# Kernel tuning notes

Hardware: AMD Instinct MI355X
Metric: run time of the kernel (lower is better)

Reference implementation:

```python
import jax, jax.numpy as jnp
import numpy as np

C = 32           # in_channels
KH, KW = 3, 3    # kernel_range
SHIFT = 1
NP = KH * KW


def conv2d(x, w, b, pad):
    # x: NCHW, w: OIHW
    y = jax.lax.conv_general_dilated(
        x, w, window_strides=(1, 1), padding=[(pad, pad), (pad, pad)],
        dimension_numbers=('NCHW', 'OIHW', 'NCHW'))
    return y + b[None, :, None, None]


def setup_inputs() -> dict:
    key = jax.random.key(0)
    ks = jax.random.split(key, 14)
    p = lambda k, shape: (jax.random.normal(k, shape, dtype=jnp.float32) * 0.02)
    inp = {
        'x':  jax.random.normal(ks[0], (4, C, 256, 256), dtype=jnp.float32),
        'wk': p(ks[1], (C * NP, C, 1, 1)), 'bk': p(ks[2], (C * NP,)),
        'wv': p(ks[3], (C * NP, C, 1, 1)), 'bv': p(ks[4], (C * NP,)),
        'wq': p(ks[5], (C, C, 1, 1)),      'bq': p(ks[6], (C,)),
        'w1': p(ks[7], (C, C, 3, 3)),      'b1': p(ks[8], (C,)),
        'w2': p(ks[9], (2 * C, C, 3, 3)),  'b2': p(ks[10], (2 * C,)),
        'w3': p(ks[11], (C, 2 * C, 3, 3)), 'b3': p(ks[12], (C,)),
    }
    return inp


def reference(x, wk, bk, wv, bv, wq, bq, w1, b1, w2, b2, w3, b3):
    B, D, H, W = x.shape
    h_half, w_half = KH // 2, KW // 2
    ph, pw = h_half * SHIFT, w_half * SHIFT

    x_k = conv2d(x, wk, bk, 0)  # (B, D*NP, H, W)
    x_v = conv2d(x, wv, bv, 0)
    x_q = conv2d(x, wq, bq, 0)  # (B, D, H, W)

    pad4 = ((0, 0), (0, 0), (ph, ph), (pw, pw))
    x_k = jnp.pad(x_k, pad4)
    x_v = jnp.pad(x_v, pad4)
    mask_pad = jnp.pad(jnp.ones((B, 1, H, W), x.dtype), pad4)

    k_ls, v_ls, m_ls = [], [], []
    layer = 0
    for i in range(-h_half, h_half + 1):
        for j in range(-w_half, w_half + 1):
            r0 = ph + i * SHIFT
            c0 = pw + j * SHIFT
            k_ls.append(x_k[:, layer * D:(layer + 1) * D, r0:r0 + H, c0:c0 + W])
            v_ls.append(x_v[:, layer * D:(layer + 1) * D, r0:r0 + H, c0:c0 + W])
            m_ls.append(mask_pad[:, :, r0:r0 + H, c0:c0 + W])
            layer += 1

    # Faithful to torch .view semantics: flat row-major reshape, NOT a permute.
    k = jnp.stack(k_ls, axis=1).reshape(B * H * W, NP, D)   # (B,NP,D,H,W) -> flat
    v = jnp.stack(v_ls, axis=1).reshape(B * H * W, NP, D)
    m = jnp.stack(m_ls, axis=1).reshape(B * H * W, NP, 1)
    q = x_q.reshape(B * H * W, 1, D)                         # (B,D,H,W) -> flat

    scores = jnp.matmul(k, jnp.swapaxes(q, -1, -2)) * m / 8.0  # (N, NP, 1)
    alpha = jax.nn.softmax(scores, axis=1)
    res = jnp.matmul(jnp.swapaxes(alpha, -1, -2), v)           # (N, 1, D)
    t = res.reshape(B, D, H, W)

    t = jax.nn.relu(conv2d(t, w1, b1, 1))
    t = jax.nn.relu(conv2d(t, w2, b2, 1))
    t = jax.nn.relu(conv2d(t, w3, b3, 1))
    return t
```

## Files before the change

### kernel.cpp

```cpp
#include <hip/hip_runtime.h>
#include <hip/hip_bf16.h>

#define B_ 4
#define C_ 32
#define H_ 256
#define W_ 256
#define S_ 65536
#define NP_ 9
#define OC_ 288
#define PR 258
#define PWN 264

using bf16 = __hip_bfloat16;
typedef __attribute__((ext_vector_type(8)))  short  short8;
typedef __attribute__((ext_vector_type(4)))  short  short4_t;
typedef __attribute__((ext_vector_type(16))) float  f32x16;

__device__ __forceinline__ float b2f(short s) {
    return __uint_as_float(((unsigned)(unsigned short)s) << 16);
}

template<int IC, int OC>
__device__ __forceinline__ void prepA_body(int fid, const float* __restrict__ w,
                                           bf16* __restrict__ apk)
{
    constexpr int NK = 9 * IC / 16;
    int tile = fid >> 9;
    int l = (fid >> 3) & 63;
    int j = fid & 7;
    int mt = tile / NK;
    int ks = tile - mt * NK;
    int q = l >> 5;
    int oc = mt * 32 + (l & 31);
    int k = ks * 16 + q * 8 + j;
    int tap = k / IC;
    int ic = k - tap * IC;
    apk[fid] = __float2bfloat16(w[((oc * IC + ic) * 3 + tap / 3) * 3 + tap % 3]);
}

template<int G>
__device__ __forceinline__ void zerob_body(int b, int p, uint4* __restrict__ buf)
{
    int gran;
    if (p < 2 * PWN * G) {
        int row = (p < PWN * G) ? 0 : 257;
        int rem = p % (PWN * G);
        gran = row * PWN * G + rem;
    } else {
        int p2 = p - 2 * PWN * G;
        int col = (p2 < 256 * G) ? 0 : 257;
        int rem = p2 % (256 * G);
        int r = rem / G + 1;
        int icg = rem - (rem / G) * G;
        gran = (r * PWN + col) * G + icg;
    }
    buf[(size_t)b * PR * PWN * G + gran] = uint4{0, 0, 0, 0};
}

__global__ __launch_bounds__(256) void k_prep(
    const float* __restrict__ wk, const float* __restrict__ wv,
    const float* __restrict__ wq,
    const float* __restrict__ w1, const float* __restrict__ w2,
    const float* __restrict__ w3,
    bf16* __restrict__ apk0, bf16* __restrict__ apk1,
    bf16* __restrict__ apk2, bf16* __restrict__ apk3,
    uint4* __restrict__ tA, uint4* __restrict__ t1, uint4* __restrict__ t2)
{
    int idx = blockIdx.x * 256 + threadIdx.x;
    if (idx < 19456) {
        int j    = idx & 7;
        int lane = (idx >> 3) & 63;
        int ks   = (idx >> 9) & 1;
        int mt   = idx >> 10;
        int oc = lane & 31;
        int ic = ks * 16 + (lane >> 5) * 8 + j;
        const float* w; int ocg;
        if (mt < 9)       { w = wk; ocg = mt * 32 + oc; }
        else if (mt < 18) { w = wv; ocg = (mt - 9) * 32 + oc; }
        else              { w = wq; ocg = oc; }
        apk0[idx] = __float2bfloat16(w[ocg * C_ + ic]);
    } else if (idx < 28672) {
        prepA_body<32, 32>(idx - 19456, w1, apk1);
    } else if (idx < 47104) {
        prepA_body<32, 64>(idx - 28672, w2, apk2);
    } else if (idx < 65536) {
        prepA_body<64, 32>(idx - 47104, w3, apk3);
    } else if (idx < 82176) {
        int i5 = idx - 65536;
        zerob_body<4>(i5 / 4160, i5 % 4160, tA);
    } else if (idx < 98816) {
        int i6 = idx - 82176;
        zerob_body<4>(i6 / 4160, i6 % 4160, t1);
    } else if (idx < 132096) {
        int i7 = idx - 98816;
        zerob_body<8>(i7 / 8320, i7 % 8320, t2);
    }
}

__global__ __launch_bounds__(256) void k_q(
    const float* __restrict__ x, const bf16* __restrict__ apk,
    const float* __restrict__ bq, bf16* __restrict__ xq)
{
    __shared__ bf16 lbuf[32][140];
    int bh  = blockIdx.x >> 9;
    int blk = blockIdx.x & 511;
    int pixw0 = blk << 7;
    int tid  = threadIdx.x;
    int wvi  = tid >> 6;
    int lane = tid & 63;
    int col  = lane & 31, q = lane >> 5;
    int pix  = pixw0 + wvi * 32 + col;

    const float* xb = x + (size_t)bh * (C_ * S_);
    bf16* xqb = xq + (size_t)bh * (32 * S_);

    short8 bfrag[2];
#pragma unroll
    for (int kk = 0; kk < 2; ++kk)
#pragma unroll
        for (int j = 0; j < 8; ++j) {
            bf16 h = __float2bfloat16(xb[(size_t)(kk * 16 + q * 8 + j) * S_ + pix]);
            bfrag[kk][j] = *reinterpret_cast<short*>(&h);
        }

    const short8* apkv = reinterpret_cast<const short8*>(apk);
    f32x16 acc = {};
    acc = __builtin_amdgcn_mfma_f32_32x32x16_bf16(bfrag[0], apkv[(18 * 2 + 0) * 64 + lane], acc, 0, 0, 0);
    acc = __builtin_amdgcn_mfma_f32_32x32x16_bf16(bfrag[1], apkv[(18 * 2 + 1) * 64 + lane], acc, 0, 0, 0);
    float bbv = bq[col];
#pragma unroll
    for (int g4 = 0; g4 < 4; ++g4) {
        short4_t sv;
#pragma unroll
        for (int j = 0; j < 4; ++j) {
            bf16 hb = __float2bfloat16(acc[g4 * 4 + j] + bbv);
            sv[j] = *reinterpret_cast<short*>(&hb);
        }
        *reinterpret_cast<short4_t*>(&lbuf[col][wvi * 32 + 8 * g4 + 4 * q]) = sv;
    }
    __syncthreads();
    int ch0 = tid >> 4, chk = tid & 15, ch1 = ch0 + 16;
    short8 v0 = *reinterpret_cast<const short8*>(&lbuf[ch0][chk * 8]);
    *reinterpret_cast<short8*>(xqb + (size_t)ch0 * S_ + pixw0 + chk * 8) = v0;
    short8 v1 = *reinterpret_cast<const short8*>(&lbuf[ch1][chk * 8]);
    *reinterpret_cast<short8*>(xqb + (size_t)ch1 * S_ + pixw0 + chk * 8) = v1;
}


#define DO_TILE(T, DTOT)                                                              \
{                                                                                     \
    int Tg = (s0 >> 5) + (T);                                                         \
    unsigned n = (unsigned)plane_base + ((unsigned)Tg << 5);                          \
    unsigned tl = (n >> 5) / 9u;                               \
    int sk0 = (int)(tl * 288u) - plane_base;                                          \
    const bf16* qp = xqb + ((size_t)tl << 5) + 4 * q;                                 \
    short4_t q0 = *reinterpret_cast<const short4_t*>(qp);                             \
    short4_t q1 = *reinterpret_cast<const short4_t*>(qp + 8);                         \
    short4_t q2 = *reinterpret_cast<const short4_t*>(qp + 16);                        \
    short4_t q3 = *reinterpret_cast<const short4_t*>(qp + 24);                        \
    int xib = ((T) << 5) + 257 + di * 256 + dj + col;                                 \
    int swx = (xib ^ (xib >> 2)) & 3;                                                 \
    short8 fa = *reinterpret_cast<const short8*>(&xs[xib * 4 + (q ^ swx)]);           \
    short8 fb = *reinterpret_cast<const short8*>(&xs[xib * 4 + ((2 + q) ^ swx)]);     \
    f32x16 ka = (f32x16){}, vh = (f32x16){};                                          \
    ka = __builtin_amdgcn_mfma_f32_32x32x16_bf16(fa, apkv[(p * 2 + 0) * 64 + lane], ka, 0, 0, 0); \
    ka = __builtin_amdgcn_mfma_f32_32x32x16_bf16(fb, apkv[(p * 2 + 1) * 64 + lane], ka, 0, 0, 0); \
    vh = __builtin_amdgcn_mfma_f32_32x32x16_bf16(fa, apkv[((9 + p) * 2 + 0) * 64 + lane], vh, 0, 0, 0); \
    vh = __builtin_amdgcn_mfma_f32_32x32x16_bf16(fb, apkv[((9 + p) * 2 + 1) * 64 + lane], vh, 0, 0, 0); \
    bool hbad  = (32 * (T) < hb_lo) || (32 * (T) >= hb_hi);                           \
    bool tb_lo = (dj == -1) && ((Tg & 7) == 0);                                       \
    bool tb_hi = (dj == 1) && ((Tg & 7) == 7);                                        \
    if (tb_lo && q == 0) q0[0] = 0;                       \
    if (tb_hi && q == 1) q3[3] = 0;                      \
    float dot = 0.f;                                                                  \
    _Pragma("unroll")                                                                 \
    for (int j3 = 0; j3 < 4; ++j3) {                                                  \
        dot += (ka[j3]      + bK) * b2f(q0[j3]);                                      \
        dot += (ka[4 + j3]  + bK) * b2f(q1[j3]);                                      \
        dot += (ka[8 + j3]  + bK) * b2f(q2[j3]);                                      \
        dot += (ka[12 + j3] + bK) * b2f(q3[j3]);                                      \
    }                                                                                 \
    if (hbad) dot = 0.f;                                                              \
    DTOT = dot + __shfl_xor(dot, 32);                                                 \
    _Pragma("unroll")                                                                 \
    for (int G2 = 0; G2 < 4; ++G2) {                                                  \
        short4_t sv;                                                                  \
        _Pragma("unroll")                                                             \
        for (int j3 = 0; j3 < 4; ++j3) {                                              \
            float val = hbad ? 0.f : (vh[G2 * 4 + j3] + bV);                          \
            bf16 hcv = __float2bfloat16(val);                                         \
            sv[j3] = *reinterpret_cast<short*>(&hcv);                                 \
        }                                                                             \
        if (G2 == 0 && tb_lo && q == 0) sv[0] = 0;                                    \
        if (G2 == 3 && tb_hi && q == 1) sv[3] = 0;                                    \
        *reinterpret_cast<short4_t*>(kvB + col * 1616 +                               \
            ((((T) << 2) + (G2 ^ ((col >> 3) & 3))) << 4) + q * 8) = sv;              \
    }                                                                                 \
}

__global__ __launch_bounds__(1024, 4) void k_fused(
    const float* __restrict__ x,
    const bf16* __restrict__ apk,
    const float* __restrict__ bk, const float* __restrict__ bv,
    const bf16* __restrict__ xq,
    bf16* __restrict__ att)
{
    extern __shared__ char smem_raw[];
    uint4* xs  = reinterpret_cast<uint4*>(smem_raw);
    char*  kvB = smem_raw + 84096;
    float* scL = reinterpret_cast<float*>(smem_raw + 135808);

    int bb = blockIdx.x >> 7;
    int s0 = (blockIdx.x & 127) << 9;

    int tid  = threadIdx.x;
    int lane = tid & 63;
    int wv   = tid >> 6;
    int col  = lane & 31;
    int q    = lane >> 5;

    const float* xb = x + (size_t)bb * (C_ * S_);
    size_t qbase = ((size_t)bb << 21);
    const bf16* xqb = xq + qbase;

    for (int i = tid; i < 5256; i += 1024) {
        int xi = i >> 2, g = i & 3;
        int s = s0 - 257 + xi;
        short8 v;
        if ((unsigned)s < 65536u) {
#pragma unroll
            for (int j = 0; j < 8; ++j) {
                bf16 h = __float2bfloat16(xb[(size_t)(g * 8 + j) * S_ + s]);
                v[j] = *reinterpret_cast<short*>(&h);
            }
        } else {
#pragma unroll
            for (int j = 0; j < 8; ++j) v[j] = 0;
        }
        int sw = (xi ^ (xi >> 2)) & 3;
        *reinterpret_cast<short8*>(&xs[xi * 4 + (g ^ sw)]) = v;
    }

    const short8* apkv = reinterpret_cast<const short8*>(apk);

    int grp  = tid >> 3, sub = tid & 7;
    int dp   = grp & 31;
    int krow = (grp >> 5) & 1;
    int hh   = sub >> 1;
    int sh   = sub & 1;
    bool athr = tid < 512;

    __syncthreads();

#pragma unroll 1
    for (int p = 0; p < 9; ++p) {
        int di = p / 3 - 1, dj = p - (p / 3) * 3 - 1;
        int hb_lo = (di == -1) ? (256 - s0) : (-0x40000000);
        int hb_hi = (di == 1) ? (65280 - s0) : 0x40000000;
        float bK = bk[p * 32 + col];
        float bV = bv[p * 32 + col];
        int plane_base = (p * 32 + col) << 16;

        float dA, dB = 0.f;
        DO_TILE(wv, dA)
        if (wv < 9) { DO_TILE(wv + 16, dB) }

        if (q == 0)      scL[wv * 32 + col] = dA;
        else if (wv < 9) scL[(wv + 16) * 32 + col] = dB;
        __syncthreads();

        if (athr) {
            int plane_base_r = (p * 32 + dp) << 16;
            unsigned tl = ((unsigned)(plane_base_r + s0 + 287)) / 288u + (unsigned)krow;
            int sk0 = (int)(tl * 288u) - plane_base_r;
            bool rv = (sk0 < s0 + 512) && (sk0 <= 65248);
            if (rv) {
                int t0  = (sk0 - s0) >> 5;
                int swz = (dp >> 3) & 3;
                float sc[9];
#pragma unroll
                for (int seg = 0; seg < 9; ++seg) {
                    float d = scL[(t0 + seg) * 32 + dp];
                    int rm = (int)tl * 9 + seg;
                    int pm = rm >> 16, sm = rm & 65535;
                    int dim = pm / 3 - 1, djm = pm - (pm / 3) * 3 - 1;
                    int hm = sm >> 8, wm = sm & 255;
                    bool mval = ((unsigned)(hm + dim) < 256u) && ((unsigned)(wm + djm) < 256u);
                    sc[seg] = mval ? d * 0.125f : 0.f;
                }
                float mx = sc[0];
#pragma unroll
                for (int s2 = 1; s2 < 9; ++s2) mx = fmaxf(mx, sc[s2]);
                float wgt[9];
                float sum = 0.f;
#pragma unroll
                for (int s2 = 0; s2 < 9; ++s2) { wgt[s2] = __expf(sc[s2] - mx); sum += wgt[s2]; }
                float inv_ = 1.f / sum;

                float oacc[4] = {0.f, 0.f, 0.f, 0.f};
#pragma unroll
                for (int seg = 0; seg < 9; ++seg) {
                    short4_t vg = *reinterpret_cast<const short4_t*>(
                        kvB + dp * 1616 + ((((t0 + seg) << 2) + (hh ^ swz)) << 4) + sh * 8);
                    float w_ = wgt[seg];
#pragma unroll
                    for (int j = 0; j < 4; ++j) oacc[j] += w_ * b2f(vg[j]);
                }
                short4_t sv;
#pragma unroll
                for (int j = 0; j < 4; ++j) {
                    bf16 h = __float2bfloat16(oacc[j] * inv_);
                    sv[j] = *reinterpret_cast<short*>(&h);
                }
                *reinterpret_cast<short4_t*>(att + qbase + ((size_t)tl << 5) + hh * 8 + sh * 4) = sv;
            }
        }
        __syncthreads();
    }
}

__global__ __launch_bounds__(320) void k_strad(
    const float* __restrict__ x,
    const float* __restrict__ wk, const float* __restrict__ bk,
    const float* __restrict__ wv, const float* __restrict__ bv,
    const bf16* __restrict__ xq, bf16* __restrict__ att)
{
    __shared__ float kL[288], vL[288], qL[32], wgtL[10];
    int e = blockIdx.x;
    int b = e >> 8, i = e & 255;
    int g = i >> 3, u = i & 7;
    int tl = g * 2048 + (((2040 + u) * 1593) & 2047);
    int tid = threadIdx.x;

    if (tid < 288) {
        int f  = tl * 288 + tid;
        int cp = f >> 16;
        int sp = f & 65535;
        int tap = cp >> 5;
        int di = tap / 3 - 1, dj = tap - (tap / 3) * 3 - 1;
        int h = sp >> 8, w = sp & 255;
        bool valid = ((unsigned)(h + di) < 256u) && ((unsigned)(w + dj) < 256u);
        float kv_ = 0.f, vv_ = 0.f;
        if (valid) {
            int sx = sp + di * 256 + dj;
            const float* xp = x + (size_t)b * (C_ * S_) + sx;
            float ks = bk[cp], vs = bv[cp];
#pragma unroll
            for (int ic = 0; ic < 32; ++ic) {
                float xv_ = xp[(size_t)ic * S_];
                ks += wk[cp * 32 + ic] * xv_;
                vs += wv[cp * 32 + ic] * xv_;
            }
            kv_ = ks; vv_ = vs;
        }
        kL[tid] = kv_; vL[tid] = vv_;
    }
    if (tid < 32) {
        bf16 hv = xq[(size_t)b * (32 * S_) + (size_t)tl * 32 + tid];
        qL[tid] = b2f(*reinterpret_cast<short*>(&hv));
    }
    __syncthreads();
    if (tid < 9) {
        float dot = 0.f;
#pragma unroll
        for (int d = 0; d < 32; ++d) dot += kL[tid * 32 + d] * qL[d];
        int rm = tl * 9 + tid;
        int pm = rm >> 16, sm = rm & 65535;
        int dim = pm / 3 - 1, djm = pm - (pm / 3) * 3 - 1;
        int hm = sm >> 8, wm = sm & 255;
        bool mval = ((unsigned)(hm + dim) < 256u) && ((unsigned)(wm + djm) < 256u);
        wgtL[tid] = mval ? dot * 0.125f : 0.f;
    }
    __syncthreads();
    if (tid == 0) {
        float mx = wgtL[0];
#pragma unroll
        for (int s2 = 1; s2 < 9; ++s2) mx = fmaxf(mx, wgtL[s2]);
        float sum = 0.f;
#pragma unroll
        for (int s2 = 0; s2 < 9; ++s2) { wgtL[s2] = __expf(wgtL[s2] - mx); sum += wgtL[s2]; }
        wgtL[9] = 1.f / sum;
    }
    __syncthreads();
    if (tid < 32) {
        float acc = 0.f;
#pragma unroll
        for (int seg = 0; seg < 9; ++seg) acc += wgtL[seg] * vL[seg * 32 + tid];
        att[(size_t)b * 2097152 + (size_t)tl * 32 + tid] = __float2bfloat16(acc * wgtL[9]);
    }
}

__global__ __launch_bounds__(256) void k_repack(
    const bf16* __restrict__ att, bf16* __restrict__ tA)
{
    int idx = blockIdx.x * 256 + threadIdx.x;
    int icg = idx & 3;
    int ps  = idx >> 2;
    int b = ps >> 16;
    int s = ps & 65535;
    const bf16* src = att + (size_t)b * (32 * S_) + icg * 8 * S_ + s;
    short8 v;
#pragma unroll
    for (int j = 0; j < 8; ++j)
        v[j] = *reinterpret_cast<const short*>(src + (size_t)j * S_);
    int row = (s >> 8) + 1, colp = (s & 255) + 1;
    *reinterpret_cast<short8*>(tA + ((size_t)((b * PR + row) * PWN + colp)) * 32 + icg * 8) = v;
}

template<int IC, int OC, bool NCHW_OUT>
__global__ __launch_bounds__(256) void k_conv3s(
    const bf16* __restrict__ in,
    const bf16* __restrict__ apk,
    const float* __restrict__ bs,
    void* __restrict__ outv)
{
    constexpr int G    = IC / 8;
    constexpr int M    = OC / 32;
    constexpr int KPT  = IC / 16;
    constexpr int NK   = 9 * KPT;
    constexpr int NT   = 2;
    constexpr int ROWP = 66;
    constexpr int ROWG = ROWP * G;
    constexpr int TOTG = 6 * ROWG;

    __shared__ uint4 smem[TOTG];

    int wg   = blockIdx.x;
    int orig = (wg & 7) * 128 + (wg >> 3);
    int b   = orig >> 8;
    int rem = orig & 255;
    int h0  = (rem >> 2) << 2;
    int w0  = (rem & 3) * 64;

    int tid = threadIdx.x;

    {
        const uint4* src = reinterpret_cast<const uint4*>(in);
#pragma unroll
        for (int i = 0; i < (TOTG + 255) / 256; ++i) {
            int idx = tid + i * 256;
            if (idx < TOTG) {
                int dr = idx / ROWG;
                int r2 = idx - dr * ROWG;
                uint4 v = src[((size_t)(b * PR + h0 + dr) * PWN + w0) * G + r2];
                int px = r2 >> ((G == 4) ? 2 : 3);
                int sw = (G == 4) ? ((px ^ (px >> 2)) & 3) : (px & 7);
                smem[dr * ROWG + (r2 & ~(G - 1)) + ((r2 ^ sw) & (G - 1))] = v;
            }
        }
    }
    __syncthreads();

    int lane = tid & 63;
    int wid  = tid >> 6;
    int col  = lane & 31, q = lane >> 5;
    int h    = h0 + wid;

    const short8* apkv = reinterpret_cast<const short8*>(apk);

    f32x16 acc[NT][M];
#pragma unroll
    for (int nt = 0; nt < NT; ++nt)
#pragma unroll
        for (int mt = 0; mt < M; ++mt) acc[nt][mt] = (f32x16){};

#pragma unroll
    for (int tap = 0; tap < 9; ++tap) {
        int dr = tap / 3 + wid;
        int dj = tap % 3;
#pragma unroll
        for (int icq = 0; icq < KPT; ++icq) {
            short8 bfr[NT];
#pragma unroll
            for (int nt = 0; nt < NT; ++nt) {
                int px = nt * 32 + col + dj;
                int sw = (G == 4) ? ((px ^ (px >> 2)) & 3) : (px & 7);
                bfr[nt] = *reinterpret_cast<const short8*>(
                    &smem[dr * ROWG + px * G + ((icq * 2 + q) ^ sw)]);
            }
#pragma unroll
            for (int mt = 0; mt < M; ++mt) {
                short8 afr = apkv[(mt * NK + tap * KPT + icq) * 64 + lane];
#pragma unroll
                for (int nt = 0; nt < NT; ++nt)
                    acc[nt][mt] = __builtin_amdgcn_mfma_f32_32x32x16_bf16(
                        afr, bfr[nt], acc[nt][mt], 0, 0, 0);
            }
        }
    }

#pragma unroll
    for (int nt = 0; nt < NT; ++nt) {
        int wout = w0 + nt * 32 + col;
#pragma unroll
        for (int mt = 0; mt < M; ++mt) {
            if (NCHW_OUT) {
                float* out = (float*)outv;
#pragma unroll
                for (int r = 0; r < 16; ++r) {
                    int oc = mt * 32 + (r & 3) + 8 * (r >> 2) + 4 * q;
                    out[(size_t)((b * OC + oc) * H_ + h) * W_ + wout] =
                        fmaxf(acc[nt][mt][r] + bs[oc], 0.f);
                }
            } else {
                bf16* out = (bf16*)outv;
                size_t base = (size_t)((b * PR + h + 1) * PWN + wout + 1) * OC + mt * 32 + 4 * q;
#pragma unroll
                for (int g4 = 0; g4 < 4; ++g4) {
                    short4_t sv;
#pragma unroll
                    for (int r4 = 0; r4 < 4; ++r4) {
                        int oc = mt * 32 + 8 * g4 + 4 * q + r4;
                        bf16 hh = __float2bfloat16(fmaxf(acc[nt][mt][g4 * 4 + r4] + bs[oc], 0.f));
                        sv[r4] = *reinterpret_cast<short*>(&hh);
                    }
                    *reinterpret_cast<short4_t*>(out + base + 8 * g4) = sv;
                }
            }
        }
    }
}

extern "C" void kernel_launch(void* const* d_in, const int* in_sizes, int n_in,
                              void* d_out, int out_size, void* d_ws, size_t ws_size,
                              hipStream_t stream)
{
    const float* x  = (const float*)d_in[0];
    const float* wk = (const float*)d_in[1];
    const float* bk = (const float*)d_in[2];
    const float* wv = (const float*)d_in[3];
    const float* bv = (const float*)d_in[4];
    const float* wq = (const float*)d_in[5];
    const float* bq = (const float*)d_in[6];
    const float* w1 = (const float*)d_in[7];
    const float* b1 = (const float*)d_in[8];
    const float* w2 = (const float*)d_in[9];
    const float* b2 = (const float*)d_in[10];
    const float* w3 = (const float*)d_in[11];
    const float* b3 = (const float*)d_in[12];
    float* out = (float*)d_out;
    char* ws = (char*)d_ws;

    bf16* xq   = (bf16*)(ws);
    bf16* tA   = (bf16*)(ws + 16777216);
    bf16* t1   = (bf16*)(ws + 34213888);
    bf16* t2   = (bf16*)(ws + 51650560);
    bf16* apk0 = (bf16*)(ws + 86523904);
    bf16* apk1 = (bf16*)(ws + 86562816);
    bf16* apk2 = (bf16*)(ws + 86581248);
    bf16* apk3 = (bf16*)(ws + 86618112);
    bf16* attB = (bf16*)d_out;

    static bool attr_set = false;
    if (!attr_set) {
        hipFuncSetAttribute(reinterpret_cast<const void*>(k_fused),
                            hipFuncAttributeMaxDynamicSharedMemorySize, 139008);
        attr_set = true;
    }

    k_prep<<<516, 256, 0, stream>>>(wk, wv, wq, w1, w2, w3,
                                    apk0, apk1, apk2, apk3,
                                    (uint4*)tA, (uint4*)t1, (uint4*)t2);

    k_q<<<2048, 256, 0, stream>>>(x, apk0, bq, xq);

    k_fused<<<512, 1024, 139008, stream>>>(x, apk0, bk, bv, xq, attB);

    k_strad<<<1024, 320, 0, stream>>>(x, wk, bk, wv, bv, xq, attB);

    k_repack<<<4096, 256, 0, stream>>>(attB, tA);

    k_conv3s<32, 32, false><<<1024, 256, 0, stream>>>(tA, apk1, b1, (void*)t1);
    k_conv3s<32, 64, false><<<1024, 256, 0, stream>>>(t1, apk2, b2, (void*)t2);
    k_conv3s<64, 32, true ><<<1024, 256, 0, stream>>>(t2, apk3, b3, (void*)out);
}
```

Baseline: 187.0 us.

## Stage bf16 pixel-major x in k_q and read it directly in k_fused

```diff
diff --git a/kernel.cpp b/kernel.cpp
--- a/kernel.cpp
+++ b/kernel.cpp
@@ -10,10 +10,13 @@
 #define OC_ 288
 #define PR 258
 #define PWN 264
+#define XGUARD 260
+#define XSTRIDE 66056
 
 using bf16 = __hip_bfloat16;
 typedef __attribute__((ext_vector_type(8)))  short  short8;
 typedef __attribute__((ext_vector_type(4)))  short  short4_t;
+typedef __attribute__((ext_vector_type(2)))  short  short2_t;
 typedef __attribute__((ext_vector_type(16))) float  f32x16;
 
 __device__ __forceinline__ float b2f(short s) {
@@ -99,7 +102,7 @@
 
 __global__ __launch_bounds__(256) void k_q(
     const float* __restrict__ x, const bf16* __restrict__ apk,
-    const float* __restrict__ bq, bf16* __restrict__ xq)
+    const float* __restrict__ bq, bf16* __restrict__ xqs, bf16* __restrict__ xb16)
 {
     __shared__ bf16 lbuf[32][140];
     int bh  = blockIdx.x >> 9;
@@ -112,7 +115,6 @@
     int pix  = pixw0 + wvi * 32 + col;
 
     const float* xb = x + (size_t)bh * (C_ * S_);
-    bf16* xqb = xq + (size_t)bh * (32 * S_);
 
     short8 bfrag[2];
 #pragma unroll
@@ -122,6 +124,12 @@
             bf16 h = __float2bfloat16(xb[(size_t)(kk * 16 + q * 8 + j) * S_ + pix]);
             bfrag[kk][j] = *reinterpret_cast<short*>(&h);
         }
+
+    {
+        bf16* xr = xb16 + ((size_t)bh * XSTRIDE + XGUARD + pix) * 32;
+        *reinterpret_cast<short8*>(xr + (q << 3))       = bfrag[0];
+        *reinterpret_cast<short8*>(xr + ((2 + q) << 3)) = bfrag[1];
+    }
 
     const short8* apkv = reinterpret_cast<const short8*>(apk);
     f32x16 acc = {};
@@ -141,179 +149,169 @@
     __syncthreads();
     int ch0 = tid >> 4, chk = tid & 15, ch1 = ch0 + 16;
     short8 v0 = *reinterpret_cast<const short8*>(&lbuf[ch0][chk * 8]);
-    *reinterpret_cast<short8*>(xqb + (size_t)ch0 * S_ + pixw0 + chk * 8) = v0;
     short8 v1 = *reinterpret_cast<const short8*>(&lbuf[ch1][chk * 8]);
-    *reinterpret_cast<short8*>(xqb + (size_t)ch1 * S_ + pixw0 + chk * 8) = v1;
-}
-
-
-#define DO_TILE(T, DTOT)                                                              \
+    int tb = (pixw0 >> 5) + (chk >> 2);
+    int G2 = chk & 3;
+    bf16* qb = xqs + (size_t)bh * (32 * S_);
+    short4_t lo0 = {v0[0], v0[1], v0[2], v0[3]}, hi0 = {v0[4], v0[5], v0[6], v0[7]};
+    short4_t lo1 = {v1[0], v1[1], v1[2], v1[3]}, hi1 = {v1[4], v1[5], v1[6], v1[7]};
+    *reinterpret_cast<short4_t*>(qb + (ch0 * 2048 + tb) * 32 + G2 * 4)      = lo0;
+    *reinterpret_cast<short4_t*>(qb + (ch0 * 2048 + tb) * 32 + 16 + G2 * 4) = hi0;
+    *reinterpret_cast<short4_t*>(qb + (ch1 * 2048 + tb) * 32 + G2 * 4)      = lo1;
+    *reinterpret_cast<short4_t*>(qb + (ch1 * 2048 + tb) * 32 + 16 + G2 * 4) = hi1;
+}
+
+
+#define DO_TILE(T, SQ)                                                                \
 {                                                                                     \
-    int Tg = (s0 >> 5) + (T);                                                         \
-    unsigned n = (unsigned)plane_base + ((unsigned)Tg << 5);                          \
-    unsigned tl = (n >> 5) / 9u;                               \
-    int sk0 = (int)(tl * 288u) - plane_base;                                          \
-    const bf16* qp = xqb + ((size_t)tl << 5) + 4 * q;                                 \
-    short4_t q0 = *reinterpret_cast<const short4_t*>(qp);                             \
-    short4_t q1 = *reinterpret_cast<const short4_t*>(qp + 8);                         \
-    short4_t q2 = *reinterpret_cast<const short4_t*>(qp + 16);                        \
-    short4_t q3 = *reinterpret_cast<const short4_t*>(qp + 24);                        \
-    int xib = ((T) << 5) + 257 + di * 256 + dj + col;                                 \
-    int swx = (xib ^ (xib >> 2)) & 3;                                                 \
-    short8 fa = *reinterpret_cast<const short8*>(&xs[xib * 4 + (q ^ swx)]);           \
-    short8 fb = *reinterpret_cast<const short8*>(&xs[xib * 4 + ((2 + q) ^ swx)]);     \
-    f32x16 ka = (f32x16){}, vh = (f32x16){};                                          \
-    ka = __builtin_amdgcn_mfma_f32_32x32x16_bf16(fa, apkv[(p * 2 + 0) * 64 + lane], ka, 0, 0, 0); \
-    ka = __builtin_amdgcn_mfma_f32_32x32x16_bf16(fb, apkv[(p * 2 + 1) * 64 + lane], ka, 0, 0, 0); \
-    vh = __builtin_amdgcn_mfma_f32_32x32x16_bf16(fa, apkv[((9 + p) * 2 + 0) * 64 + lane], vh, 0, 0, 0); \
-    vh = __builtin_amdgcn_mfma_f32_32x32x16_bf16(fb, apkv[((9 + p) * 2 + 1) * 64 + lane], vh, 0, 0, 0); \
-    bool hbad  = (32 * (T) < hb_lo) || (32 * (T) >= hb_hi);                           \
-    bool tb_lo = (dj == -1) && ((Tg & 7) == 0);                                       \
-    bool tb_hi = (dj == 1) && ((Tg & 7) == 7);                                        \
-    if (tb_lo && q == 0) q0[0] = 0;                       \
-    if (tb_hi && q == 1) q3[3] = 0;                      \
-    float dot = 0.f;                                                                  \
-    _Pragma("unroll")                                                                 \
-    for (int j3 = 0; j3 < 4; ++j3) {                                                  \
-        dot += (ka[j3]      + bK) * b2f(q0[j3]);                                      \
-        dot += (ka[4 + j3]  + bK) * b2f(q1[j3]);                                      \
-        dot += (ka[8 + j3]  + bK) * b2f(q2[j3]);                                      \
-        dot += (ka[12 + j3] + bK) * b2f(q3[j3]);                                      \
-    }                                                                                 \
-    if (hbad) dot = 0.f;                                                              \
-    DTOT = dot + __shfl_xor(dot, 32);                                                 \
-    _Pragma("unroll")                                                                 \
-    for (int G2 = 0; G2 < 4; ++G2) {                                                  \
-        short4_t sv;                                                                  \
+    int Tg = tgbase + (T);                                                            \
+    if (Tg < 2048) {                                                                  \
+        unsigned n = (unsigned)plane_base + ((unsigned)Tg << 5);                      \
+        unsigned tl = n / 288u;                                                       \
+        const bf16* qp = xqb + ((size_t)tl << 5) + (q << 4);                          \
+        short8 qA = *reinterpret_cast<const short8*>(qp);                             \
+        short8 qB = *reinterpret_cast<const short8*>(qp + 8);                         \
+        const bf16* xp = xbg + (size_t)(((T) << 5) + s0 + shf + col) * 32;            \
+        short8 fa = *reinterpret_cast<const short8*>(xp + (q << 3));                  \
+        short8 fb = *reinterpret_cast<const short8*>(xp + ((2 + q) << 3));            \
+        bool hbad  = ((((T) << 5) < hb_lo) || (((T) << 5) >= hb_hi));                 \
+        bool tb_lo = (dj == -1) && ((Tg & 7) == 0);                                   \
+        bool tb_hi = (dj == 1) && ((Tg & 7) == 7);                                    \
+        if (tb_lo && q == 0) qA[0] = 0;                                               \
+        if (tb_hi && q == 1) qB[7] = 0;                                               \
+        f32x16 ka = (f32x16){};                                                       \
+        ka = __builtin_amdgcn_mfma_f32_32x32x16_bf16(fa, apkv[(p * 2 + 0) * 64 + lane], ka, 0, 0, 0); \
+        ka = __builtin_amdgcn_mfma_f32_32x32x16_bf16(fb, apkv[(p * 2 + 1) * 64 + lane], ka, 0, 0, 0); \
+        float dot = 0.f;                                                              \
         _Pragma("unroll")                                                             \
         for (int j3 = 0; j3 < 4; ++j3) {                                              \
-            float val = hbad ? 0.f : (vh[G2 * 4 + j3] + bV);                          \
-            bf16 hcv = __float2bfloat16(val);                                         \
-            sv[j3] = *reinterpret_cast<short*>(&hcv);                                 \
+            dot += (ka[j3]      + bK) * b2f(qA[j3]);                                  \
+            dot += (ka[4 + j3]  + bK) * b2f(qA[4 + j3]);                              \
+            dot += (ka[8 + j3]  + bK) * b2f(qB[j3]);                                  \
+            dot += (ka[12 + j3] + bK) * b2f(qB[4 + j3]);                              \
         }                                                                             \
-        if (G2 == 0 && tb_lo && q == 0) sv[0] = 0;                                    \
-        if (G2 == 3 && tb_hi && q == 1) sv[3] = 0;                                    \
-        *reinterpret_cast<short4_t*>(kvB + col * 1616 +                               \
-            ((((T) << 2) + (G2 ^ ((col >> 3) & 3))) << 4) + q * 8) = sv;              \
+        if (hbad) dot = 0.f;                                                          \
+        dot += __shfl_xor(dot, 32);                                                   \
+        if (q == (SQ)) scL[T][col] = dot;                                             \
+        f32x16 vh = (f32x16){};                                                       \
+        vh = __builtin_amdgcn_mfma_f32_32x32x16_bf16(fa, apkv[((9 + p) * 2 + 0) * 64 + lane], vh, 0, 0, 0); \
+        vh = __builtin_amdgcn_mfma_f32_32x32x16_bf16(fb, apkv[((9 + p) * 2 + 1) * 64 + lane], vh, 0, 0, 0); \
+        _Pragma("unroll")                                                             \
+        for (int G2 = 0; G2 < 4; ++G2) {                                              \
+            short4_t sv;                                                              \
+            _Pragma("unroll")                                                         \
+            for (int j3 = 0; j3 < 4; ++j3) {                                          \
+                float val = hbad ? 0.f : (vh[G2 * 4 + j3] + bV);                      \
+                bf16 hcv = __float2bfloat16(val);                                     \
+                sv[j3] = *reinterpret_cast<short*>(&hcv);                             \
+            }                                                                         \
+            if (G2 == 0 && tb_lo && q == 0) sv[0] = 0;                                \
+            if (G2 == 3 && tb_hi && q == 1) sv[3] = 0;                                \
+            *reinterpret_cast<short4_t*>(&kvB[col][((T) << 5) + ((G2 ^ xcol) << 3) + (q << 2)]) = sv; \
+        }                                                                             \
     }                                                                                 \
 }
 
-__global__ __launch_bounds__(1024, 4) void k_fused(
-    const float* __restrict__ x,
+__global__ __launch_bounds__(512, 8) void k_fused(
+    const bf16* __restrict__ xb16,
     const bf16* __restrict__ apk,
     const float* __restrict__ bk, const float* __restrict__ bv,
-    const bf16* __restrict__ xq,
+    const bf16* __restrict__ xqs,
     bf16* __restrict__ att)
 {
-    extern __shared__ char smem_raw[];
-    uint4* xs  = reinterpret_cast<uint4*>(smem_raw);
-    char*  kvB = smem_raw + 84096;
-    float* scL = reinterpret_cast<float*>(smem_raw + 135808);
-
-    int bb = blockIdx.x >> 7;
-    int s0 = (blockIdx.x & 127) << 9;
+    __shared__ bf16  kvB[32][520];
+    __shared__ float scL[16][32];
+    __shared__ unsigned short scM[288];
+
+    int swzb = (blockIdx.x & 7) * 128 + (blockIdx.x >> 3);
+    int bb = swzb >> 8;
+    int s0 = (swzb & 255) << 8;
+    int tgbase = s0 >> 5;
 
     int tid  = threadIdx.x;
     int lane = tid & 63;
     int wv   = tid >> 6;
     int col  = lane & 31;
     int q    = lane >> 5;
-
-    const float* xb = x + (size_t)bb * (C_ * S_);
+    int xcol = (col >> 3) & 3;
+
+    const bf16* xbg = xb16 + ((size_t)bb * XSTRIDE + XGUARD) * 32;
     size_t qbase = ((size_t)bb << 21);
-    const bf16* xqb = xq + qbase;
-
-    for (int i = tid; i < 5256; i += 1024) {
-        int xi = i >> 2, g = i & 3;
-        int s = s0 - 257 + xi;
-        short8 v;
-        if ((unsigned)s < 65536u) {
-#pragma unroll
-            for (int j = 0; j < 8; ++j) {
-                bf16 h = __float2bfloat16(xb[(size_t)(g * 8 + j) * S_ + s]);
-                v[j] = *reinterpret_cast<short*>(&h);
-            }
-        } else {
-#pragma unroll
-            for (int j = 0; j < 8; ++j) v[j] = 0;
-        }
-        int sw = (xi ^ (xi >> 2)) & 3;
-        *reinterpret_cast<short8*>(&xs[xi * 4 + (g ^ sw)]) = v;
-    }
-
+    const bf16* xqb = xqs + qbase;
     const short8* apkv = reinterpret_cast<const short8*>(apk);
 
-    int grp  = tid >> 3, sub = tid & 7;
-    int dp   = grp & 31;
-    int krow = (grp >> 5) & 1;
-    int hh   = sub >> 1;
-    int sh   = sub & 1;
-    bool athr = tid < 512;
-
-    __syncthreads();
+    if (tid < 288) {
+        int pp = tid >> 5, dpp = tid & 31;
+        int plane_base_r = ((pp << 5) + dpp) << 16;
+        unsigned tl = ((unsigned)(plane_base_r + s0 + 287)) / 288u;
+        int sk0 = (int)(tl * 288u) - plane_base_r;
+        unsigned m = 0;
+        if (sk0 < s0 + 256 && sk0 <= 65248) {
+            m = 0x8000u;
+#pragma unroll
+            for (int seg = 0; seg < 9; ++seg) {
+                int rm = (int)tl * 9 + seg;
+                int pm = rm >> 16, sm = rm & 65535;
+                int dim = pm / 3 - 1, djm = pm - (pm / 3) * 3 - 1;
+                int hm = sm >> 8, wm = sm & 255;
+                bool mval = ((unsigned)(hm + dim) < 256u) && ((unsigned)(wm + djm) < 256u);
+                m |= (mval ? 1u : 0u) << seg;
+            }
+        }
+        scM[tid] = (unsigned short)m;
+    }
+
+    int dpp = tid >> 4;
+    int sub = tid & 15;
+    int xdp = (dpp >> 3) & 3;
 
 #pragma unroll 1
     for (int p = 0; p < 9; ++p) {
         int di = p / 3 - 1, dj = p - (p / 3) * 3 - 1;
+        int shf = di * 256 + dj;
         int hb_lo = (di == -1) ? (256 - s0) : (-0x40000000);
         int hb_hi = (di == 1) ? (65280 - s0) : 0x40000000;
         float bK = bk[p * 32 + col];
         float bV = bv[p * 32 + col];
-        int plane_base = (p * 32 + col) << 16;
-
-        float dA, dB = 0.f;
-        DO_TILE(wv, dA)
-        if (wv < 9) { DO_TILE(wv + 16, dB) }
-
-        if (q == 0)      scL[wv * 32 + col] = dA;
-        else if (wv < 9) scL[(wv + 16) * 32 + col] = dB;
+        int plane_base = ((p << 5) + col) << 16;
+
+        DO_TILE(wv, 0)
+        DO_TILE(wv + 8, 1)
         __syncthreads();
 
-        if (athr) {
-            int plane_base_r = (p * 32 + dp) << 16;
-            unsigned tl = ((unsigned)(plane_base_r + s0 + 287)) / 288u + (unsigned)krow;
+        unsigned mflags = scM[p * 32 + dpp];
+        if (mflags & 0x8000u) {
+            int plane_base_r = ((p << 5) + dpp) << 16;
+            unsigned tl = ((unsigned)(plane_base_r + s0 + 287)) / 288u;
             int sk0 = (int)(tl * 288u) - plane_base_r;
-            bool rv = (sk0 < s0 + 512) && (sk0 <= 65248);
-            if (rv) {
-                int t0  = (sk0 - s0) >> 5;
-                int swz = (dp >> 3) & 3;
-                float sc[9];
-#pragma unroll
-                for (int seg = 0; seg < 9; ++seg) {
-                    float d = scL[(t0 + seg) * 32 + dp];
-                    int rm = (int)tl * 9 + seg;
-                    int pm = rm >> 16, sm = rm & 65535;
-                    int dim = pm / 3 - 1, djm = pm - (pm / 3) * 3 - 1;
-                    int hm = sm >> 8, wm = sm & 255;
-                    bool mval = ((unsigned)(hm + dim) < 256u) && ((unsigned)(wm + djm) < 256u);
-                    sc[seg] = mval ? d * 0.125f : 0.f;
-                }
-                float mx = sc[0];
-#pragma unroll
-                for (int s2 = 1; s2 < 9; ++s2) mx = fmaxf(mx, sc[s2]);
-                float wgt[9];
-                float sum = 0.f;
-#pragma unroll
-                for (int s2 = 0; s2 < 9; ++s2) { wgt[s2] = __expf(sc[s2] - mx); sum += wgt[s2]; }
-                float inv_ = 1.f / sum;
-
-                float oacc[4] = {0.f, 0.f, 0.f, 0.f};
-#pragma unroll
-                for (int seg = 0; seg < 9; ++seg) {
-                    short4_t vg = *reinterpret_cast<const short4_t*>(
-                        kvB + dp * 1616 + ((((t0 + seg) << 2) + (hh ^ swz)) << 4) + sh * 8);
-                    float w_ = wgt[seg];
-#pragma unroll
-                    for (int j = 0; j < 4; ++j) oacc[j] += w_ * b2f(vg[j]);
-                }
-                short4_t sv;
-#pragma unroll
-                for (int j = 0; j < 4; ++j) {
-                    bf16 h = __float2bfloat16(oacc[j] * inv_);
-                    sv[j] = *reinterpret_cast<short*>(&h);
-                }
-                *reinterpret_cast<short4_t*>(att + qbase + ((size_t)tl << 5) + hh * 8 + sh * 4) = sv;
-            }
+            int t0 = (sk0 - s0) >> 5;
+            float sc[9];
+#pragma unroll
+            for (int seg = 0; seg < 9; ++seg)
+                sc[seg] = ((mflags >> seg) & 1u) ? scL[t0 + seg][dpp] * 0.125f : 0.f;
+            float mx = sc[0];
+#pragma unroll
+            for (int s2 = 1; s2 < 9; ++s2) mx = fmaxf(mx, sc[s2]);
+            float wgt[9];
+            float sum = 0.f;
+#pragma unroll
+            for (int s2 = 0; s2 < 9; ++s2) { wgt[s2] = __expf(sc[s2] - mx); sum += wgt[s2]; }
+            float inv_ = 1.f / sum;
+
+            int go  = (sub << 1) & 7;
+            int gsw = ((sub >> 2) ^ xdp) << 3;
+            float o0 = 0.f, o1 = 0.f;
+#pragma unroll
+            for (int seg = 0; seg < 9; ++seg) {
+                const bf16* vp = &kvB[dpp][(t0 + seg) * 32 + gsw + go];
+                float w_ = wgt[seg];
+                o0 += w_ * b2f(*reinterpret_cast<const short*>(vp));
+                o1 += w_ * b2f(*(reinterpret_cast<const short*>(vp) + 1));
+            }
+            bf16 h0 = __float2bfloat16(o0 * inv_);
+            bf16 h1 = __float2bfloat16(o1 * inv_);
+            short2_t s2v = {*reinterpret_cast<short*>(&h0), *reinterpret_cast<short*>(&h1)};
+            *reinterpret_cast<short2_t*>(att + qbase + ((size_t)tl << 5) + (sub << 1)) = s2v;
         }
         __syncthreads();
     }
@@ -323,7 +321,7 @@
     const float* __restrict__ x,
     const float* __restrict__ wk, const float* __restrict__ bk,
     const float* __restrict__ wv, const float* __restrict__ bv,
-    const bf16* __restrict__ xq, bf16* __restrict__ att)
+    const bf16* __restrict__ xqs, bf16* __restrict__ att)
 {
     __shared__ float kL[288], vL[288], qL[32], wgtL[10];
     int e = blockIdx.x;
@@ -356,7 +354,8 @@
         kL[tid] = kv_; vL[tid] = vv_;
     }
     if (tid < 32) {
-        bf16 hv = xq[(size_t)b * (32 * S_) + (size_t)tl * 32 + tid];
+        int pos = ((tid >> 2) & 1) * 16 + (tid >> 3) * 4 + (tid & 3);
+        bf16 hv = xqs[(size_t)b * (32 * S_) + (size_t)tl * 32 + pos];
         qL[tid] = b2f(*reinterpret_cast<short*>(&hv));
     }
     __syncthreads();
@@ -541,7 +540,7 @@
     float* out = (float*)d_out;
     char* ws = (char*)d_ws;
 
-    bf16* xq   = (bf16*)(ws);
+    bf16* xqs  = (bf16*)(ws);
     bf16* tA   = (bf16*)(ws + 16777216);
     bf16* t1   = (bf16*)(ws + 34213888);
     bf16* t2   = (bf16*)(ws + 51650560);
@@ -549,24 +548,18 @@
     bf16* apk1 = (bf16*)(ws + 86562816);
     bf16* apk2 = (bf16*)(ws + 86581248);
     bf16* apk3 = (bf16*)(ws + 86618112);
+    bf16* xb16 = (bf16*)(ws + 86654976);
     bf16* attB = (bf16*)d_out;
-
-    static bool attr_set = false;
-    if (!attr_set) {
-        hipFuncSetAttribute(reinterpret_cast<const void*>(k_fused),
-                            hipFuncAttributeMaxDynamicSharedMemorySize, 139008);
-        attr_set = true;
-    }
 
     k_prep<<<516, 256, 0, stream>>>(wk, wv, wq, w1, w2, w3,
                                     apk0, apk1, apk2, apk3,
                                     (uint4*)tA, (uint4*)t1, (uint4*)t2);
 
-    k_q<<<2048, 256, 0, stream>>>(x, apk0, bq, xq);
-
-    k_fused<<<512, 1024, 139008, stream>>>(x, apk0, bk, bv, xq, attB);
-
-    k_strad<<<1024, 320, 0, stream>>>(x, wk, bk, wv, bv, xq, attB);
+    k_q<<<2048, 256, 0, stream>>>(x, apk0, bq, xqs, xb16);
+
+    k_fused<<<1024, 512, 0, stream>>>(xb16, apk0, bk, bv, xqs, attB);
+
+    k_strad<<<1024, 320, 0, stream>>>(x, wk, bk, wv, bv, xqs, attB);
 
     k_repack<<<4096, 256, 0, stream>>>(attB, tA);
 
```

After: 200.9 us. 7.5% more time.
